# Optimization experiments

Measured on AMD Instinct MI355X. Metric: run time of the kernel, lower is better.

Reference implementation:

```python
import jax, jax.numpy as jnp
import numpy as np

B, C, H, W = 2, 256, 64, 64
NH, HD, K = 4, 64, 16  # num_head, head_channel, n_clusters
N = H * W
SCALE = HD ** 0.5


def _lin(x, Wm, b):
    return x @ Wm + b


def _mlp(x, W1, b1, W2, b2):
    h = _lin(x, W1, b1)
    h = jnp.where(h > 0, h, 0.01 * h)  # LeakyReLU(0.01)
    return _lin(h, W2, b2)  # dropout p=0.0 -> identity


def setup_inputs() -> dict:
    key = jax.random.key(0)
    ks = jax.random.split(key, 20)
    s = 1.0 / np.sqrt(C)
    s2 = 1.0 / np.sqrt(2 * C)
    inp = {
        "q_img": jax.random.normal(ks[0], (B, C, H, W), jnp.float32),
        "k_img_map": jax.random.normal(ks[1], (B, C, H, W), jnp.float32),
        "v_img_map": jax.random.normal(ks[2], (B, C, H, W), jnp.float32),
        "labels": jax.random.randint(ks[3], (B, H, W), 0, K),
        "pixel_coefficients": jax.random.uniform(ks[4], (B, N, N), jnp.float32),
        "Wq": jax.random.uniform(ks[5], (C, C), jnp.float32, -s, s),
        "bq": jnp.zeros((C,), jnp.float32),
        "Wk": jax.random.uniform(ks[6], (C, C), jnp.float32, -s, s),
        "bk": jnp.zeros((C,), jnp.float32),
        "Wv": jax.random.uniform(ks[7], (C, C), jnp.float32, -s, s),
        "bv": jnp.zeros((C,), jnp.float32),
        "W11": jax.random.uniform(ks[8], (C, 2 * C), jnp.float32, -s, s),
        "b11": jnp.zeros((2 * C,), jnp.float32),
        "W12": jax.random.uniform(ks[9], (2 * C, C), jnp.float32, -s2, s2),
        "b12": jnp.zeros((C,), jnp.float32),
        "W21": jax.random.uniform(ks[10], (C, 2 * C), jnp.float32, -s, s),
        "b21": jnp.zeros((2 * C,), jnp.float32),
        "W22": jax.random.uniform(ks[11], (2 * C, C), jnp.float32, -s2, s2),
        "b22": jnp.zeros((C,), jnp.float32),
    }
    return inp


def reference(q_img, k_img_map, v_img_map, labels, pixel_coefficients,
              Wq, bq, Wk, bk, Wv, bv, W11, b11, W12, b12, W21, b21, W22, b22):
    # [B,C,H,W] -> [B,N,C]
    q = _lin(q_img.transpose(0, 2, 3, 1).reshape(B, N, C), Wq, bq)
    k = _lin(k_img_map.transpose(0, 2, 3, 1).reshape(B, N, C), Wk, bk)
    v = _lin(v_img_map.transpose(0, 2, 3, 1).reshape(B, N, C), Wv, bv)

    lab = labels.reshape(B, N)
    onehot = (lab[:, :, None] == jnp.arange(K)[None, None, :]).astype(jnp.float32)  # [B,N,K]
    num_k = jnp.einsum('bnk,bnc->bkc', onehot, k)
    den_k = onehot.sum(axis=1)[:, :, None] + 1e-6
    centers_k = num_k / den_k  # [B,K,C]

    qm = q.reshape(B, N, NH, HD).transpose(0, 2, 1, 3)  # [B,h,N,d]
    km = k.reshape(B, N, NH, HD).transpose(0, 2, 1, 3)
    vm = v.reshape(B, N, NH, HD).transpose(0, 2, 1, 3)
    cm = centers_k.reshape(B, K, NH, HD).transpose(0, 2, 1, 3)  # [B,h,K,d]

    attn_intra = jnp.einsum('bhnd,bhmd->bhnm', qm, km)          # [B,h,N,N]
    attn_centers = jnp.einsum('bhnd,bhkd->bhnk', qm, cm)        # [B,h,N,K]

    same = (lab[:, :, None] == lab[:, None, :])[:, None]        # [B,1,N,N]
    idx = jnp.broadcast_to(lab[:, None, None, :], (B, NH, N, N))
    attn_inter = jnp.take_along_axis(attn_centers, idx, axis=-1) * pixel_coefficients[:, None]

    scores = jnp.where(same, attn_intra, attn_inter) / SCALE
    attn = jax.nn.softmax(scores, axis=-1)
    out = jnp.einsum('bhnm,bhmd->bhnd', attn, vm).transpose(0, 2, 1, 3).reshape(B, N, C)

    rs1 = v + _mlp(out, W11, b11, W12, b12)        # [B,N,C] (v_spatial residual)
    rs2 = rs1 + _mlp(rs1, W21, b21, W22, b22)
    return rs2.reshape(B, H, W, C).transpose(0, 3, 1, 2)  # [B,C,H,W]
```

## Files before the change

### kernel.cpp

```cpp
#include <hip/hip_runtime.h>
#include <stdint.h>

#define Bv 2
#define Cv 256
#define Nv 4096
#define NHv 4
#define HDv 64
#define Kv 16


typedef __attribute__((ext_vector_type(8))) short bf16x8;
typedef __attribute__((ext_vector_type(4))) float f32x4;

__device__ __forceinline__ float bf2f(unsigned short u) {
  union { unsigned int i; float f; } x; x.i = ((unsigned int)u) << 16; return x.f;
}
__device__ __forceinline__ unsigned short f2bf(float f) {
  union { float f; unsigned int i; } x; x.f = f;
  unsigned int r = x.i + 0x7FFF + ((x.i >> 16) & 1);
  return (unsigned short)(r >> 16);
}
__device__ __forceinline__ unsigned int cvt_pk_bf16(float lo, float hi) {
  unsigned int r;
  asm("v_cvt_pk_bf16_f32 %0, %1, %2" : "=v"(r) : "v"(lo), "v"(hi));
  return r;
}
__device__ __forceinline__ float exp2_raw(float x) {
  float r;
  asm("v_exp_f32 %0, %1" : "=v"(r) : "v"(x));
  return r;
}

__global__ __launch_bounds__(256) void imgt_k(
    const float* __restrict__ qi, const float* __restrict__ ki,
    const float* __restrict__ vi, unsigned short* __restrict__ dst)
{
  const int z = blockIdx.z;
  const float* src = (z < 2 ? qi : (z < 4 ? ki : vi)) + (long long)(z & 1) * Cv * Nv;
  unsigned short* out = dst + (long long)z * Nv * Cv;
  __shared__ float t[32][33];
  const int x = threadIdx.x, y = threadIdx.y;
  const int n0 = blockIdx.x * 32, c0 = blockIdx.y * 32;
  for (int i = y; i < 32; i += 8)
    t[i][x] = src[(long long)(c0 + i) * Nv + n0 + x];
  __syncthreads();
  for (int i = y; i < 32; i += 8)
    out[(long long)(n0 + i) * Cv + c0 + x] = f2bf(t[x][i]);
}

struct WP { const float* p[7]; };

__global__ __launch_bounds__(256) void wt_k(WP wp, unsigned short* __restrict__ dst)
{
  const int z = blockIdx.z;
  const int KD[7] = {256, 256, 256, 256, 512, 256, 512};
  const int ND[7] = {256, 256, 256, 512, 256, 512, 256};
  const long long OFF[7] = {0, 65536, 131072, 196608, 327680, 458752, 589824};
  const int Kw = KD[z], Nw = ND[z];
  const int nb = blockIdx.x * 32, kb2 = blockIdx.y * 32;
  if (nb >= Nw || kb2 >= Kw) return;
  __shared__ float t[32][33];
  const int x = threadIdx.x, y = threadIdx.y;
  const float* src = wp.p[z];
  for (int i = y; i < 32; i += 8)
    t[i][x] = src[(long long)(kb2 + i) * Nw + nb + x];
  __syncthreads();
  for (int i = y; i < 32; i += 8)
    dst[OFF[z] + (long long)(nb + i) * Kw + kb2 + x] = f2bf(t[x][i]);
}

__global__ __launch_bounds__(256) void proj64_k(
    const unsigned short* __restrict__ imgT, const unsigned short* __restrict__ wt,
    const float* __restrict__ bq, const float* __restrict__ bk, const float* __restrict__ bv,
    unsigned short* __restrict__ qbf, unsigned short* __restrict__ kbf,
    float* __restrict__ vpp, unsigned short* __restrict__ vtb)
{
  __shared__ __align__(16) unsigned short As[64][72];
  __shared__ __align__(16) unsigned short Bs[64][72];
  const int tid = threadIdx.x;
  const int w = tid >> 6, lane = tid & 63;
  const int lr = lane & 15, quad = lane >> 4;
  const int m0 = blockIdx.x * 64, n0 = blockIdx.y * 64;
  const int z = blockIdx.z, zz = z >> 1, bb = z & 1;
  const int wm = (w >> 1) * 32, wn = (w & 1) * 32;
  const int sr = tid >> 2, sh = (tid & 3) * 16;
  const long long NvCv = (long long)Nv * Cv;

  const float* bias = zz == 0 ? bq : (zz == 1 ? bk : bv);
  const unsigned short* Ab0 = imgT + (long long)z * NvCv + (long long)(m0 + sr) * Cv + sh;
  const unsigned short* Bb0 = wt + (long long)zz * 65536 + (long long)(n0 + sr) * Cv + sh;

  f32x4 acc[2][2];
#pragma unroll
  for (int i = 0; i < 2; ++i)
#pragma unroll
    for (int j = 0; j < 2; ++j) acc[i][j] = (f32x4){0.f, 0.f, 0.f, 0.f};

  uint4 rA0 = *(const uint4*)Ab0, rA1 = *(const uint4*)(Ab0 + 8);
  uint4 rB0 = *(const uint4*)Bb0, rB1 = *(const uint4*)(Bb0 + 8);

  for (int k0 = 0; k0 < Cv; k0 += 64) {
    *(uint4*)&As[sr][sh] = rA0; *(uint4*)&As[sr][sh + 8] = rA1;
    *(uint4*)&Bs[sr][sh] = rB0; *(uint4*)&Bs[sr][sh + 8] = rB1;
    __syncthreads();
    if (k0 + 64 < Cv) {
      rA0 = *(const uint4*)(Ab0 + k0 + 64); rA1 = *(const uint4*)(Ab0 + k0 + 72);
      rB0 = *(const uint4*)(Bb0 + k0 + 64); rB1 = *(const uint4*)(Bb0 + k0 + 72);
    }
#pragma unroll
    for (int ks = 0; ks < 2; ++ks) {
      bf16x8 af[2], bfr[2];
#pragma unroll
      for (int i = 0; i < 2; ++i)
        af[i] = *(const bf16x8*)&As[wm + i * 16 + lr][ks * 32 + quad * 8];
#pragma unroll
      for (int j = 0; j < 2; ++j)
        bfr[j] = *(const bf16x8*)&Bs[wn + j * 16 + lr][ks * 32 + quad * 8];
#pragma unroll
      for (int i = 0; i < 2; ++i)
#pragma unroll
        for (int j = 0; j < 2; ++j)
          acc[i][j] = __builtin_amdgcn_mfma_f32_16x16x32_bf16(af[i], bfr[j], acc[i][j], 0, 0, 0);
    }
    __syncthreads();
  }

#pragma unroll
  for (int j = 0; j < 2; ++j) {
    const int col = n0 + wn + j * 16 + lr;
    const float bvv = bias[col];
#pragma unroll
    for (int i = 0; i < 2; ++i) {
      const int mb = m0 + wm + i * 16 + quad * 4;
      float r[4];
#pragma unroll
      for (int reg = 0; reg < 4; ++reg) r[reg] = acc[i][j][reg] + bvv;
      const long long ob = (long long)bb * NvCv;
      if (zz == 0) {
#pragma unroll
        for (int reg = 0; reg < 4; ++reg)
          qbf[ob + (long long)(mb + reg) * Cv + col] = f2bf(r[reg] * 0.18033688f);
      } else if (zz == 1) {
#pragma unroll
        for (int reg = 0; reg < 4; ++reg)
          kbf[ob + (long long)(mb + reg) * Cv + col] = f2bf(r[reg]);
      } else {
#pragma unroll
        for (int reg = 0; reg < 4; ++reg)
          vpp[ob + (long long)(mb + reg) * Cv + col] = r[reg];
        uint2 pk;
        pk.x = cvt_pk_bf16(r[0], r[1]);
        pk.y = cvt_pk_bf16(r[2], r[3]);
        *(uint2*)&vtb[ob + (long long)col * Nv + mb] = pk;
      }
    }
  }
}

template<bool ABF16, int ACT, int RES, int OM>
__global__ __launch_bounds__(256) void mm64_k(
    const void* __restrict__ A, const unsigned short* __restrict__ Bt,
    const float* __restrict__ bias, const float* __restrict__ Res,
    float* __restrict__ outF, unsigned short* __restrict__ outB,
    int M, int Nn, int Kd)
{
  __shared__ __align__(16) unsigned short As[64][72];
  __shared__ __align__(16) unsigned short Bs[64][72];
  const int tid = threadIdx.x;
  const int w = tid >> 6, lane = tid & 63;
  const int lr = lane & 15, quad = lane >> 4;
  const int m0 = blockIdx.x * 64, n0 = blockIdx.y * 64;
  const int wm = (w >> 1) * 32, wn = (w & 1) * 32;
  const int sr = tid >> 2, sh = (tid & 3) * 16;

  f32x4 acc[2][2];
#pragma unroll
  for (int i = 0; i < 2; ++i)
#pragma unroll
    for (int j = 0; j < 2; ++j) acc[i][j] = (f32x4){0.f, 0.f, 0.f, 0.f};

  const long long abase = (long long)(m0 + sr) * Kd + sh;
  const unsigned short* Bb = Bt + (long long)(n0 + sr) * Kd + sh;

  uint4 rA0, rA1, rB0, rB1;
  float4 fA[4];
  if (ABF16) {
    const unsigned short* Ab = (const unsigned short*)A + abase;
    rA0 = *(const uint4*)Ab; rA1 = *(const uint4*)(Ab + 8);
  } else {
    const float* Af = (const float*)A + abase;
    fA[0] = *(const float4*)Af;      fA[1] = *(const float4*)(Af + 4);
    fA[2] = *(const float4*)(Af + 8); fA[3] = *(const float4*)(Af + 12);
  }
  rB0 = *(const uint4*)Bb; rB1 = *(const uint4*)(Bb + 8);

  for (int k0 = 0; k0 < Kd; k0 += 64) {
    if (ABF16) {
      *(uint4*)&As[sr][sh] = rA0; *(uint4*)&As[sr][sh + 8] = rA1;
    } else {
#pragma unroll
      for (int t = 0; t < 2; ++t) {
        uint4 pk;
        pk.x = cvt_pk_bf16(fA[t * 2].x, fA[t * 2].y);
        pk.y = cvt_pk_bf16(fA[t * 2].z, fA[t * 2].w);
        pk.z = cvt_pk_bf16(fA[t * 2 + 1].x, fA[t * 2 + 1].y);
        pk.w = cvt_pk_bf16(fA[t * 2 + 1].z, fA[t * 2 + 1].w);
        *(uint4*)&As[sr][sh + t * 8] = pk;
      }
    }
    *(uint4*)&Bs[sr][sh] = rB0; *(uint4*)&Bs[sr][sh + 8] = rB1;
    __syncthreads();
    if (k0 + 64 < Kd) {
      if (ABF16) {
        const unsigned short* Ab = (const unsigned short*)A + abase + k0 + 64;
        rA0 = *(const uint4*)Ab; rA1 = *(const uint4*)(Ab + 8);
      } else {
        const float* Af = (const float*)A + abase + k0 + 64;
        fA[0] = *(const float4*)Af;      fA[1] = *(const float4*)(Af + 4);
        fA[2] = *(const float4*)(Af + 8); fA[3] = *(const float4*)(Af + 12);
      }
      rB0 = *(const uint4*)(Bb + k0 + 64); rB1 = *(const uint4*)(Bb + k0 + 72);
    }
#pragma unroll
    for (int ks = 0; ks < 2; ++ks) {
      bf16x8 af[2], bfr[2];
#pragma unroll
      for (int i = 0; i < 2; ++i)
        af[i] = *(const bf16x8*)&As[wm + i * 16 + lr][ks * 32 + quad * 8];
#pragma unroll
      for (int j = 0; j < 2; ++j)
        bfr[j] = *(const bf16x8*)&Bs[wn + j * 16 + lr][ks * 32 + quad * 8];
#pragma unroll
      for (int i = 0; i < 2; ++i)
#pragma unroll
        for (int j = 0; j < 2; ++j)
          acc[i][j] = __builtin_amdgcn_mfma_f32_16x16x32_bf16(af[i], bfr[j], acc[i][j], 0, 0, 0);
    }
    __syncthreads();
  }

#pragma unroll
  for (int j = 0; j < 2; ++j) {
    const int col = n0 + wn + j * 16 + lr;
    const float bv = bias[col];
#pragma unroll
    for (int i = 0; i < 2; ++i) {
      const int mb = m0 + wm + i * 16 + quad * 4;
      float r[4];
#pragma unroll
      for (int reg = 0; reg < 4; ++reg) {
        float v = acc[i][j][reg] + bv;
        if (ACT) v = v > 0.f ? v : 0.01f * v;
        if (RES) v += Res[(long long)(mb + reg) * Nn + col];
        r[reg] = v;
      }
      if (OM == 0) {
#pragma unroll
        for (int reg = 0; reg < 4; ++reg)
          outF[(long long)(mb + reg) * Nn + col] = r[reg];
      } else if (OM == 1) {
#pragma unroll
        for (int reg = 0; reg < 4; ++reg)
          outB[(long long)(mb + reg) * Nn + col] = f2bf(r[reg]);
      } else {
        const float4 st = {r[0], r[1], r[2], r[3]};
        *(float4*)&outF[((long long)((mb >> 12) * Cv + col)) * Nv + (mb & 4095)] = st;
      }
    }
  }
}

__global__ __launch_bounds__(256) void zero_k(float* p, int n)
{
  const int i = blockIdx.x * 256 + threadIdx.x;
  if (i < n) p[i] = 0.f;
}

__global__ __launch_bounds__(256) void center_accum(
    const unsigned short* __restrict__ kb, const int* __restrict__ labels,
    float* __restrict__ cent, float* __restrict__ cnts)
{
  __shared__ int lab_s[512];
  const int bx = blockIdx.x;
  const int chunk = bx & 7;
  const int kk = (bx >> 3) & 15;
  const int b = bx >> 7;
  const int c = threadIdx.x;
  const int nbase = chunk * 512;
  for (int i = threadIdx.x; i < 512; i += 256) lab_s[i] = labels[b * Nv + nbase + i];
  __syncthreads();
  float acc = 0.f;
  int cnt = 0;
#pragma unroll 4
  for (int i = 0; i < 512; ++i) {
    if (lab_s[i] == kk) {
      acc += bf2f(kb[(long long)(b * Nv + nbase + i) * Cv + c]);
      ++cnt;
    }
  }
  atomicAdd(&cent[(b * Kv + kk) * Cv + c], acc);
  if (c == 0) atomicAdd(&cnts[b * Kv + kk], (float)cnt);
}

__global__ __launch_bounds__(256) void center_norm(float* cent, const float* cnts)
{
  const int i = blockIdx.x * 256 + threadIdx.x;
  cent[i] = cent[i] / (cnts[i >> 8] + 1e-6f);
}

union PSCS {
  unsigned short p[4][16][68];
  float c[16][68];
};

__global__ __launch_bounds__(256) void attn_k(
    const unsigned short* __restrict__ qb, const unsigned short* __restrict__ kb,
    const unsigned short* __restrict__ vtb, const float* __restrict__ cent,
    const int* __restrict__ labels, const float* __restrict__ pc,
    float* __restrict__ opart, float* __restrict__ lpart)
{
  __shared__ __align__(16) unsigned short q_s[64][72];
  __shared__ __align__(16) unsigned short k_s[64][72];
  __shared__ __align__(16) unsigned short vt_s[64][72];
  __shared__ __align__(16) PSCS u_s;
  __shared__ float ac_s[64][17];

  const int tid = threadIdx.x;
  const int lane = tid & 63, w = tid >> 6;
  const int lr = lane & 15, quad = lane >> 4;
  const int bx = blockIdx.x;
  const int qt = bx & 63, h = (bx >> 6) & 3, b = (bx >> 8) & 1;
  const int part = bx >> 9;
  const int n0 = qt * 64;
  const int mbase = part * 2048;
  const int sr2 = tid >> 2, so2 = (tid & 3) * 16;
  const int row_l = w * 16 + quad * 4;
  const long long pcb = (long long)b * Nv * Nv;

  {
    const unsigned short* src = qb + ((long long)(b * Nv + n0 + sr2)) * Cv + h * HDv + so2;
    *(uint4*)&q_s[sr2][so2] = *(const uint4*)src;
    *(uint4*)&q_s[sr2][so2 + 8] = *(const uint4*)(src + 8);
  }
  for (int idx = tid; idx < Kv * HDv; idx += 256)
    u_s.c[idx >> 6][idx & 63] = cent[((long long)(b * Kv + (idx >> 6))) * Cv + h * HDv + (idx & 63)];

  const unsigned short* kub = kb + ((long long)(b * Nv + mbase)) * Cv + h * HDv;
  const unsigned short* vub = vtb + ((long long)(b * Cv + h * HDv)) * Nv + mbase;
  const int koff = sr2 * Cv + so2;
  const int voff = sr2 * Nv + so2;
  const int* lbp = labels + b * Nv + mbase + lr;
  const float* pcp[4];
#pragma unroll
  for (int reg = 0; reg < 4; ++reg)
    pcp[reg] = pc + pcb + (long long)(n0 + row_l + reg) * Nv + mbase + lr;

  uint4 ka0, ka1, va0, va1;
  float pc1[4][4];
  int labm1[4], labq[4];
  ka0 = *(const uint4*)(kub + koff); ka1 = *(const uint4*)(kub + koff + 8);
  va0 = *(const uint4*)(vub + voff); va1 = *(const uint4*)(vub + voff + 8);
  kub += 64 * Cv; vub += 64;
#pragma unroll
  for (int sub = 0; sub < 4; ++sub) {
    labm1[sub] = lbp[sub * 16];
#pragma unroll
    for (int reg = 0; reg < 4; ++reg)
      pc1[sub][reg] = pcp[reg][sub * 16];
  }
  lbp += 64;
#pragma unroll
  for (int reg = 0; reg < 4; ++reg) pcp[reg] += 64;
#pragma unroll
  for (int reg = 0; reg < 4; ++reg) labq[reg] = labels[b * Nv + n0 + row_l + reg];

  __syncthreads();
  for (int idx = tid; idx < 64 * Kv; idx += 256) {
    const int r = idx >> 4, kk = idx & 15;
    float s = 0.f;
#pragma unroll
    for (int d = 0; d < HDv; ++d) s += bf2f(q_s[r][d]) * u_s.c[kk][d];
    ac_s[r][kk] = s;
  }
  const bf16x8 qa0 = *(const bf16x8*)&q_s[w * 16 + lr][quad * 8];
  const bf16x8 qa1 = *(const bf16x8*)&q_s[w * 16 + lr][32 + quad * 8];
  __syncthreads();

  float acg[4][4];
#pragma unroll
  for (int sub = 0; sub < 4; ++sub)
#pragma unroll
    for (int reg = 0; reg < 4; ++reg)
      acg[sub][reg] = ac_s[row_l + reg][labm1[sub]];

  *(uint4*)&k_s[sr2][so2] = ka0; *(uint4*)&k_s[sr2][so2 + 8] = ka1;
  *(uint4*)&vt_s[sr2][so2] = va0; *(uint4*)&vt_s[sr2][so2 + 8] = va1;
  __syncthreads();

  f32x4 oacc[4];
#pragma unroll
  for (int s2 = 0; s2 < 4; ++s2) oacc[s2] = (f32x4){0.f, 0.f, 0.f, 0.f};
  float lrow[4] = {0.f, 0.f, 0.f, 0.f};

  for (int t = 0; t < 32; ++t) {
    const bool has = (t < 31);

    if (has) {
      ka0 = *(const uint4*)(kub + koff); ka1 = *(const uint4*)(kub + koff + 8);
      va0 = *(const uint4*)(vub + voff); va1 = *(const uint4*)(vub + voff + 8);
      kub += 64 * Cv; vub += 64;
    }

    f32x4 sacc[4];
    __builtin_amdgcn_s_setprio(1);
#pragma unroll
    for (int sub = 0; sub < 4; ++sub) {
      const bf16x8 kb0 = *(const bf16x8*)&k_s[sub * 16 + lr][quad * 8];
      const bf16x8 kb1 = *(const bf16x8*)&k_s[sub * 16 + lr][32 + quad * 8];
      f32x4 s = (f32x4){0.f, 0.f, 0.f, 0.f};
      s = __builtin_amdgcn_mfma_f32_16x16x32_bf16(qa0, kb0, s, 0, 0, 0);
      s = __builtin_amdgcn_mfma_f32_16x16x32_bf16(qa1, kb1, s, 0, 0, 0);
      sacc[sub] = s;
    }
    __builtin_amdgcn_s_setprio(0);

#pragma unroll
    for (int sub = 0; sub < 4; ++sub) {
      float p4[4];
#pragma unroll
      for (int reg = 0; reg < 4; ++reg) {
        const float s = (labm1[sub] == labq[reg]) ? sacc[sub][reg]
                                                  : acg[sub][reg] * pc1[sub][reg];
        const float p = exp2_raw(s);
        lrow[reg] += p;
        p4[reg] = p;
      }
      const unsigned int pk01 = cvt_pk_bf16(p4[0], p4[1]);
      const unsigned int pk23 = cvt_pk_bf16(p4[2], p4[3]);
      unsigned short* pp = &u_s.p[w][quad * 4][sub * 16 + lr];
      pp[0]   = (unsigned short)pk01;
      pp[68]  = (unsigned short)(pk01 >> 16);
      pp[136] = (unsigned short)pk23;
      pp[204] = (unsigned short)(pk23 >> 16);
    }

    if (has) {
#pragma unroll
      for (int sub = 0; sub < 4; ++sub) {
        labm1[sub] = lbp[sub * 16];
#pragma unroll
        for (int reg = 0; reg < 4; ++reg)
          pc1[sub][reg] = pcp[reg][sub * 16];
      }
      lbp += 64;
#pragma unroll
      for (int reg = 0; reg < 4; ++reg) pcp[reg] += 64;
    }

    const bf16x8 pa0 = *(const bf16x8*)&u_s.p[w][lr][quad * 8];
    const bf16x8 pa1 = *(const bf16x8*)&u_s.p[w][lr][32 + quad * 8];
    __builtin_amdgcn_s_setprio(1);
#pragma unroll
    for (int sub = 0; sub < 4; ++sub) {
      const bf16x8 vb0 = *(const bf16x8*)&vt_s[sub * 16 + lr][quad * 8];
      const bf16x8 vb1 = *(const bf16x8*)&vt_s[sub * 16 + lr][32 + quad * 8];
      oacc[sub] = __builtin_amdgcn_mfma_f32_16x16x32_bf16(pa0, vb0, oacc[sub], 0, 0, 0);
      oacc[sub] = __builtin_amdgcn_mfma_f32_16x16x32_bf16(pa1, vb1, oacc[sub], 0, 0, 0);
    }
    __builtin_amdgcn_s_setprio(0);

    if (has) {
#pragma unroll
      for (int sub = 0; sub < 4; ++sub)
#pragma unroll
        for (int reg = 0; reg < 4; ++reg)
          acg[sub][reg] = ac_s[row_l + reg][labm1[sub]];
    }

    __syncthreads();
    if (has) {
      *(uint4*)&k_s[sr2][so2] = ka0; *(uint4*)&k_s[sr2][so2 + 8] = ka1;
      *(uint4*)&vt_s[sr2][so2] = va0; *(uint4*)&vt_s[sr2][so2 + 8] = va1;
    }
    __syncthreads();
  }

#pragma unroll
  for (int reg = 0; reg < 4; ++reg) {
    float l = lrow[reg];
    l += __shfl_xor(l, 1); l += __shfl_xor(l, 2);
    l += __shfl_xor(l, 4); l += __shfl_xor(l, 8);
    const int row = n0 + row_l + reg;
    const long long obase = (long long)part * 2097152 + ((long long)(b * Nv + row)) * Cv + h * HDv;
#pragma unroll
    for (int sub = 0; sub < 4; ++sub)
      opart[obase + sub * 16 + lr] = oacc[sub][reg];
    if (lr == 0)
      lpart[part * 32768 + (b * 4 + h) * 4096 + row] = l;
  }
}

__global__ __launch_bounds__(256) void combine_k(
    const float* __restrict__ op, const float* __restrict__ lp,
    unsigned short* __restrict__ aob)
{
  const long long i4 = ((long long)blockIdx.x * 256 + threadIdx.x) * 4;
  const int c = (int)(i4 & 255), n = (int)((i4 >> 8) & 4095), b = (int)(i4 >> 20);
  const int h = c >> 6;
  const float l = lp[(b * 4 + h) * 4096 + n] + lp[32768 + (b * 4 + h) * 4096 + n];
  const float inv = 1.f / l;
  const float4 a = *(const float4*)&op[i4];
  const float4 d = *(const float4*)&op[2097152 + i4];
  uint2 pk;
  pk.x = cvt_pk_bf16((a.x + d.x) * inv, (a.y + d.y) * inv);
  pk.y = cvt_pk_bf16((a.z + d.z) * inv, (a.w + d.w) * inv);
  *(uint2*)&aob[i4] = pk;
}

extern "C" void kernel_launch(void* const* d_in, const int* in_sizes, int n_in,
                              void* d_out, int out_size, void* d_ws, size_t ws_size,
                              hipStream_t stream)
{
  const float* q_img = (const float*)d_in[0];
  const float* k_img = (const float*)d_in[1];
  const float* v_img = (const float*)d_in[2];
  const int* labels  = (const int*)d_in[3];
  const float* pc    = (const float*)d_in[4];
  const float* Wq  = (const float*)d_in[5];  const float* bq  = (const float*)d_in[6];
  const float* Wk  = (const float*)d_in[7];  const float* bk  = (const float*)d_in[8];
  const float* Wv  = (const float*)d_in[9];  const float* bv  = (const float*)d_in[10];
  const float* W11 = (const float*)d_in[11]; const float* b11 = (const float*)d_in[12];
  const float* W12 = (const float*)d_in[13]; const float* b12 = (const float*)d_in[14];
  const float* W21 = (const float*)d_in[15]; const float* b21 = (const float*)d_in[16];
  const float* W22 = (const float*)d_in[17]; const float* b22 = (const float*)d_in[18];
  float* outp = (float*)d_out;

  const long long SZ = (long long)Bv * Nv * Cv;
  float* ws    = (float*)d_ws;
  float* vpp   = ws;
  float* rs1   = vpp + SZ;
  float* opart = rs1 + SZ;
  float* lpart = opart + 2 * SZ;
  float* cent  = lpart + 65536;
  float* cnts  = cent + Bv * Kv * Cv;
  unsigned short* wt   = (unsigned short*)(cnts + Bv * Kv);
  unsigned short* qbf  = wt + 720896;
  unsigned short* kbf  = qbf + SZ;
  unsigned short* vtb  = kbf + SZ;
  unsigned short* aob  = vtb + SZ;
  unsigned short* h1b  = aob + SZ;
  unsigned short* imgT = aob;

  imgt_k<<<dim3(Nv / 32, Cv / 32, 6), dim3(32, 8), 0, stream>>>(q_img, k_img, v_img, imgT);
  WP wp = {{Wq, Wk, Wv, W11, W12, W21, W22}};
  wt_k<<<dim3(16, 16, 7), dim3(32, 8), 0, stream>>>(wp, wt);

  proj64_k<<<dim3(64, 4, 6), 256, 0, stream>>>(imgT, wt, bq, bk, bv, qbf, kbf, vpp, vtb);

  zero_k<<<dim3(33), 256, 0, stream>>>(cent, Bv * Kv * Cv + Bv * Kv);
  center_accum<<<dim3(Bv * Kv * 8), 256, 0, stream>>>(kbf, labels, cent, cnts);
  center_norm<<<dim3(Bv * Kv * Cv / 256), 256, 0, stream>>>(cent, cnts);

  attn_k<<<dim3(1024), 256, 0, stream>>>(qbf, kbf, vtb, cent, labels, pc, opart, lpart);
  combine_k<<<dim3(2048), 256, 0, stream>>>(opart, lpart, aob);

  mm64_k<true, 1, 0, 1><<<dim3(128, 8), 256, 0, stream>>>(
      aob, wt + 196608, b11, nullptr, nullptr, h1b, 2 * Nv, 2 * Cv, Cv);
  mm64_k<true, 0, 1, 0><<<dim3(128, 4), 256, 0, stream>>>(
      h1b, wt + 327680, b12, vpp, rs1, nullptr, 2 * Nv, Cv, 2 * Cv);

  mm64_k<false, 1, 0, 1><<<dim3(128, 8), 256, 0, stream>>>(
      rs1, wt + 458752, b21, nullptr, nullptr, h1b, 2 * Nv, 2 * Cv, Cv);
  mm64_k<true, 0, 1, 4><<<dim3(128, 4), 256, 0, stream>>>(
      h1b, wt + 589824, b22, rs1, outp, nullptr, 2 * Nv, Cv, 2 * Cv);
}
```

Baseline: 407.0 us.

## Use bpermute for center-score gather and emit bf16 copy of rs1 in epilogue

In the attention kernel, each lane now caches its own center-score value and fetches the label-indexed one from other lanes with ds_bpermute, replacing a label-indexed LDS gather from ac_s. Global address arithmetic is recomputed per tile instead of carried in incremented pointers. The second MLP matmul now writes rs1 as both fp32 and bf16 (new OM==2 mode), so the next matmul can take bf16 input instead of converting from fp32. This adds an extra bf16 store in one epilogue and relies on the bpermute index layout lining up with the MFMA row mapping.

After: 403.6 us. Within noise of the previous version (-0.8%).

```diff
diff --git a/kernel.cpp b/kernel.cpp
--- a/kernel.cpp
+++ b/kernel.cpp
@@ -29,6 +29,9 @@
   float r;
   asm("v_exp_f32 %0, %1" : "=v"(r) : "v"(x));
   return r;
+}
+__device__ __forceinline__ float bperm_f(int idx_bytes, float v) {
+  return __int_as_float(__builtin_amdgcn_ds_bpermute(idx_bytes, __float_as_int(v)));
 }
 
 __global__ __launch_bounds__(256) void imgt_k(
@@ -262,6 +265,12 @@
 #pragma unroll
         for (int reg = 0; reg < 4; ++reg)
           outB[(long long)(mb + reg) * Nn + col] = f2bf(r[reg]);
+      } else if (OM == 2) {
+#pragma unroll
+        for (int reg = 0; reg < 4; ++reg) {
+          outF[(long long)(mb + reg) * Nn + col] = r[reg];
+          outB[(long long)(mb + reg) * Nn + col] = f2bf(r[reg]);
+        }
       } else {
         const float4 st = {r[0], r[1], r[2], r[3]};
         *(float4*)&outF[((long long)((mb >> 12) * Cv + col)) * Nv + (mb & 4095)] = st;
@@ -345,32 +354,22 @@
   for (int idx = tid; idx < Kv * HDv; idx += 256)
     u_s.c[idx >> 6][idx & 63] = cent[((long long)(b * Kv + (idx >> 6))) * Cv + h * HDv + (idx & 63)];
 
-  const unsigned short* kub = kb + ((long long)(b * Nv + mbase)) * Cv + h * HDv;
-  const unsigned short* vub = vtb + ((long long)(b * Cv + h * HDv)) * Nv + mbase;
-  const int koff = sr2 * Cv + so2;
-  const int voff = sr2 * Nv + so2;
-  const int* lbp = labels + b * Nv + mbase + lr;
-  const float* pcp[4];
-#pragma unroll
-  for (int reg = 0; reg < 4; ++reg)
-    pcp[reg] = pc + pcb + (long long)(n0 + row_l + reg) * Nv + mbase + lr;
-
   uint4 ka0, ka1, va0, va1;
   float pc1[4][4];
   int labm1[4], labq[4];
-  ka0 = *(const uint4*)(kub + koff); ka1 = *(const uint4*)(kub + koff + 8);
-  va0 = *(const uint4*)(vub + voff); va1 = *(const uint4*)(vub + voff + 8);
-  kub += 64 * Cv; vub += 64;
+  {
+    const long long ks = ((long long)(b * Nv + mbase + sr2)) * Cv + h * HDv + so2;
+    ka0 = *(const uint4*)(kb + ks); ka1 = *(const uint4*)(kb + ks + 8);
+    const long long vs = ((long long)(b * Cv + h * HDv + sr2)) * Nv + mbase + so2;
+    va0 = *(const uint4*)(vtb + vs); va1 = *(const uint4*)(vtb + vs + 8);
+  }
 #pragma unroll
   for (int sub = 0; sub < 4; ++sub) {
-    labm1[sub] = lbp[sub * 16];
+    labm1[sub] = labels[b * Nv + mbase + sub * 16 + lr];
 #pragma unroll
     for (int reg = 0; reg < 4; ++reg)
-      pc1[sub][reg] = pcp[reg][sub * 16];
-  }
-  lbp += 64;
-#pragma unroll
-  for (int reg = 0; reg < 4; ++reg) pcp[reg] += 64;
+      pc1[sub][reg] = pc[pcb + (long long)(n0 + row_l + reg) * Nv + mbase + sub * 16 + lr];
+  }
 #pragma unroll
   for (int reg = 0; reg < 4; ++reg) labq[reg] = labels[b * Nv + n0 + row_l + reg];
 
@@ -386,12 +385,18 @@
   const bf16x8 qa1 = *(const bf16x8*)&q_s[w * 16 + lr][32 + quad * 8];
   __syncthreads();
 
+  float acv[4];
+#pragma unroll
+  for (int reg = 0; reg < 4; ++reg) acv[reg] = ac_s[w * 16 + quad * 4 + reg][lr];
+
   float acg[4][4];
 #pragma unroll
-  for (int sub = 0; sub < 4; ++sub)
+  for (int sub = 0; sub < 4; ++sub) {
+    const int bidx = (quad << 6) + (labm1[sub] << 2);
 #pragma unroll
     for (int reg = 0; reg < 4; ++reg)
-      acg[sub][reg] = ac_s[row_l + reg][labm1[sub]];
+      acg[sub][reg] = bperm_f(bidx, acv[reg]);
+  }
 
   *(uint4*)&k_s[sr2][so2] = ka0; *(uint4*)&k_s[sr2][so2 + 8] = ka1;
   *(uint4*)&vt_s[sr2][so2] = va0; *(uint4*)&vt_s[sr2][so2 + 8] = va1;
@@ -403,12 +408,14 @@
   float lrow[4] = {0.f, 0.f, 0.f, 0.f};
 
   for (int t = 0; t < 32; ++t) {
+    const int m0 = mbase + t * 64;
     const bool has = (t < 31);
 
     if (has) {
-      ka0 = *(const uint4*)(kub + koff); ka1 = *(const uint4*)(kub + koff + 8);
-      va0 = *(const uint4*)(vub + voff); va1 = *(const uint4*)(vub + voff + 8);
-      kub += 64 * Cv; vub += 64;
+      const long long ks = ((long long)(b * Nv + m0 + 64 + sr2)) * Cv + h * HDv + so2;
+      ka0 = *(const uint4*)(kb + ks); ka1 = *(const uint4*)(kb + ks + 8);
+      const long long vs = ((long long)(b * Cv + h * HDv + sr2)) * Nv + m0 + 64 + so2;
+      va0 = *(const uint4*)(vtb + vs); va1 = *(const uint4*)(vtb + vs + 8);
     }
 
     f32x4 sacc[4];
@@ -447,14 +454,11 @@
     if (has) {
 #pragma unroll
       for (int sub = 0; sub < 4; ++sub) {
-        labm1[sub] = lbp[sub * 16];
-#pragma unroll
-        for (int reg = 0; reg < 4; ++reg)
-          pc1[sub][reg] = pcp[reg][sub * 16];
-      }
-      lbp += 64;
-#pragma unroll
-      for (int reg = 0; reg < 4; ++reg) pcp[reg] += 64;
+        labm1[sub] = labels[b * Nv + m0 + 64 + sub * 16 + lr];
+#pragma unroll
+        for (int reg = 0; reg < 4; ++reg)
+          pc1[sub][reg] = pc[pcb + (long long)(n0 + row_l + reg) * Nv + m0 + 64 + sub * 16 + lr];
+      }
     }
 
     const bf16x8 pa0 = *(const bf16x8*)&u_s.p[w][lr][quad * 8];
@@ -471,10 +475,12 @@
 
     if (has) {
 #pragma unroll
-      for (int sub = 0; sub < 4; ++sub)
-#pragma unroll
-        for (int reg = 0; reg < 4; ++reg)
-          acg[sub][reg] = ac_s[row_l + reg][labm1[sub]];
+      for (int sub = 0; sub < 4; ++sub) {
+        const int bidx = (quad << 6) + (labm1[sub] << 2);
+#pragma unroll
+        for (int reg = 0; reg < 4; ++reg)
+          acg[sub][reg] = bperm_f(bidx, acv[reg]);
+      }
     }
 
     __syncthreads();
@@ -566,11 +572,11 @@
 
   mm64_k<true, 1, 0, 1><<<dim3(128, 8), 256, 0, stream>>>(
       aob, wt + 196608, b11, nullptr, nullptr, h1b, 2 * Nv, 2 * Cv, Cv);
-  mm64_k<true, 0, 1, 0><<<dim3(128, 4), 256, 0, stream>>>(
-      h1b, wt + 327680, b12, vpp, rs1, nullptr, 2 * Nv, Cv, 2 * Cv);
-
-  mm64_k<false, 1, 0, 1><<<dim3(128, 8), 256, 0, stream>>>(
-      rs1, wt + 458752, b21, nullptr, nullptr, h1b, 2 * Nv, 2 * Cv, Cv);
+  mm64_k<true, 0, 1, 2><<<dim3(128, 4), 256, 0, stream>>>(
+      h1b, wt + 327680, b12, vpp, rs1, aob, 2 * Nv, Cv, 2 * Cv);
+
+  mm64_k<true, 1, 0, 1><<<dim3(128, 8), 256, 0, stream>>>(
+      aob, wt + 458752, b21, nullptr, nullptr, h1b, 2 * Nv, 2 * Cv, Cv);
   mm64_k<true, 0, 1, 4><<<dim3(128, 4), 256, 0, stream>>>(
       h1b, wt + 589824, b22, rs1, outp, nullptr, 2 * Nv, Cv, 2 * Cv);
 }
```
